# Kernel optimization log

Measured on AMD Instinct MI355X. Metric: run time of the kernel, lower is better.

The kernel has to match this reference:

```python
import jax, jax.numpy as jnp
import numpy as np

CHNN = 1024
K = 2048


def _conv1x1(W, b, x):
    # x: (B, C_in, L), W: (C_out, C_in), b: (C_out,)
    return jnp.einsum('oc,bcl->bol', W, x) + b[None, :, None]


def setup_inputs() -> dict:
    key = jax.random.key(0)
    ks = jax.random.split(key, 10)
    s = 0.02
    return {
        'vc': jax.random.normal(ks[0], (1, CHNN, K), dtype=jnp.float32),
        'vm': jax.random.normal(ks[1], (1, CHNN, K), dtype=jnp.float32),
        'W_ak': jax.random.normal(ks[2], (K, CHNN), dtype=jnp.float32) * s,
        'b_ak': jax.random.normal(ks[3], (K,), dtype=jnp.float32) * s,
        'W_c': jax.random.normal(ks[4], (CHNN, CHNN), dtype=jnp.float32) * s,
        'b_c': jax.random.normal(ks[5], (CHNN,), dtype=jnp.float32) * s,
        'W_mad': jax.random.normal(ks[6], (CHNN, CHNN), dtype=jnp.float32) * s,
        'b_mad': jax.random.normal(ks[7], (CHNN,), dtype=jnp.float32) * s,
        'W_gcn': jax.random.normal(ks[8], (CHNN, CHNN), dtype=jnp.float32) * s,
        'b_gcn': jax.random.normal(ks[9], (CHNN,), dtype=jnp.float32) * s,
    }


def reference(vc, vm, W_ak, b_ak, W_c, b_c, W_mad, b_mad, W_gcn, b_gcn):
    # vcw: (1, K, L) assignment logits; softmax over the K (channel) dim
    vcw = _conv1x1(W_ak, b_ak, vc)
    vcw = jax.nn.softmax(vcw, axis=1)
    w = vcw[0].T                      # (L, K)  (batch forced to 1 by squeeze(0))
    # vm features: (1, CHNN, K)
    vmr = jax.nn.relu(_conv1x1(W_c, b_c, vm))
    # F.linear(vm, w): contract last dim (K) with w's second dim -> (1, CHNN, L)
    vma = jnp.einsum('bck,lk->bcl', vmr, w)
    vma = _conv1x1(W_mad, b_mad, vma)  # (1, CHNN, L)
    # dense adjacency over positions: (1, L, L)
    A = jnp.einsum('bck,bcl->bkl', vma, vma)
    # GCN: x (1, K, CHNN) @ W + b, then softmax(A) @ x  (requires L == K)
    x = jnp.swapaxes(vmr, 1, 2) @ W_gcn + b_gcn
    A = jax.nn.softmax(A, axis=-1)
    out = A @ x                        # (1, L, CHNN)
    return jnp.swapaxes(out, 1, 2)     # (1, CHNN, L)
```

## Files before the change

### kernel.cpp

```cpp
#include <hip/hip_runtime.h>
#include <hip/hip_bf16.h>


typedef __bf16 bf16x4 __attribute__((ext_vector_type(4)));
typedef __bf16 bf16x8 __attribute__((ext_vector_type(8)));
typedef float  f32x4  __attribute__((ext_vector_type(4)));

typedef const void __attribute__((address_space(1)))* gptr_t;
typedef void       __attribute__((address_space(3)))* lptr_t;

__device__ __forceinline__ void load16_lds(const __bf16* g, __bf16* l)
{
    __builtin_amdgcn_global_load_lds((gptr_t)g, (lptr_t)l, 16, 0, 0);
}

#define WAITCNT_VM16 0x4F70
#define WAITCNT_VM8  0x0F78
#define WAITCNT_VM0  0x0F70

template<typename OT, int BIAS_, bool RELU_, int STORE_>
struct GC {
    using OUT_T = OT;
    static constexpr int BIAS = BIAS_, STORE = STORE_;
    static constexpr bool RELU = RELU_;
};

template<class CF>
__device__ __forceinline__ void gemm_body(
    int bid, __bf16* sA, __bf16* sB,
    const __bf16* __restrict__ A, const __bf16* __restrict__ B,
    const float* __restrict__ bias,
    typename CF::OUT_T* __restrict__ C, typename CF::OUT_T* __restrict__ CT,
    int M, int N, int K, int ntx)
{
    const int lane = threadIdx.x & 63;
    const int m0 = (bid / ntx) * 64, n0 = (bid % ntx) * 64;
    const __bf16* gA = A + (size_t)m0 * K;
    const __bf16* gB = B + (size_t)n0 * K;

    f32x4 acc[4][4];
    #pragma unroll
    for (int i = 0; i < 4; ++i)
        #pragma unroll
        for (int j = 0; j < 4; ++j)
            acc[i][j] = (f32x4){0.f, 0.f, 0.f, 0.f};

    auto stage = [&](int k0, int buf) {
        #pragma unroll
        for (int i = 0; i < 4; ++i) {
            const int c = i * 64 + lane;
            const int s = (c ^ (c >> 2) ^ (c >> 4)) & 3;
            load16_lds(gA + (size_t)(c >> 2) * K + k0 + s * 8,
                       &sA[buf * 2048 + i * 512]);
        }
        #pragma unroll
        for (int i = 0; i < 4; ++i) {
            const int c = i * 64 + lane;
            const int s = (c ^ (c >> 2) ^ (c >> 4)) & 3;
            load16_lds(gB + (size_t)(c >> 2) * K + k0 + s * 8,
                       &sB[buf * 2048 + i * 512]);
        }
    };

    const int fsw = ((lane >> 4) ^ lane ^ (lane >> 2)) & 3;

    auto compute = [&](int buf) {
        bf16x8 af[4], bfr[4];
        #pragma unroll
        for (int i = 0; i < 4; ++i) {
            const int off = buf * 2048 + (i * 16 + (lane & 15)) * 32 + fsw * 8;
            af[i]  = *(const bf16x8*)&sA[off];
            bfr[i] = *(const bf16x8*)&sB[off];
        }
        #pragma unroll
        for (int i = 0; i < 4; ++i)
            #pragma unroll
            for (int j = 0; j < 4; ++j)
                acc[i][j] = __builtin_amdgcn_mfma_f32_16x16x32_bf16(af[i], bfr[j], acc[i][j], 0, 0, 0);
    };

    stage(0, 0);
    stage(32, 1);
    stage(64, 2);
    int cur = 0;
    for (int k0 = 0; k0 < K - 96; k0 += 32) {
        __builtin_amdgcn_s_waitcnt(WAITCNT_VM16);
        compute(cur);
        stage(k0 + 96, cur);
        cur = (cur == 2) ? 0 : cur + 1;
    }
    __builtin_amdgcn_s_waitcnt(WAITCNT_VM16);
    compute(cur); cur = (cur == 2) ? 0 : cur + 1;
    __builtin_amdgcn_s_waitcnt(WAITCNT_VM8);
    compute(cur); cur = (cur == 2) ? 0 : cur + 1;
    __builtin_amdgcn_s_waitcnt(WAITCNT_VM0);
    compute(cur);

    #pragma unroll
    for (int i = 0; i < 4; ++i) {
        const int rowb = m0 + i * 16 + (lane >> 4) * 4;
        #pragma unroll
        for (int j = 0; j < 4; ++j) {
            const int col = n0 + j * 16 + (lane & 15);
            f32x4 v = acc[i][j];
            #pragma unroll
            for (int r = 0; r < 4; ++r) {
                float f = v[r];
                if (CF::BIAS == 1) f += bias[rowb + r];
                if (CF::BIAS == 2) f += bias[col];
                if (CF::RELU) f = fmaxf(f, 0.f);
                v[r] = f;
            }
            if (CF::STORE == 0) {
                #pragma unroll
                for (int r = 0; r < 4; ++r)
                    C[(size_t)(rowb + r) * N + col] = (typename CF::OUT_T)v[r];
            } else {
                if constexpr (sizeof(typename CF::OUT_T) == 4) {
                    *(f32x4*)&CT[(size_t)col * M + rowb] = v;
                } else {
                    bf16x4 w = { (__bf16)v[0], (__bf16)v[1], (__bf16)v[2], (__bf16)v[3] };
                    *(bf16x4*)&CT[(size_t)col * M + rowb] = w;
                }
            }
        }
    }
}

__device__ __forceinline__ void softmax_row_w(__bf16* __restrict__ p)
{
    const int lane = threadIdx.x & 63;
    bf16x8 v[4];
    float f[32];
    #pragma unroll
    for (int r = 0; r < 4; ++r)
        v[r] = *(const bf16x8*)&p[(r * 64 + lane) * 8];
    float m = -1e30f;
    #pragma unroll
    for (int r = 0; r < 4; ++r)
        #pragma unroll
        for (int j = 0; j < 8; ++j) {
            f[r * 8 + j] = (float)v[r][j];
            m = fmaxf(m, f[r * 8 + j]);
        }
    #pragma unroll
    for (int s = 1; s < 64; s <<= 1) m = fmaxf(m, __shfl_xor(m, s, 64));
    float sum = 0.f;
    #pragma unroll
    for (int i = 0; i < 32; ++i) { f[i] = expf(f[i] - m); sum += f[i]; }
    #pragma unroll
    for (int s = 1; s < 64; s <<= 1) sum += __shfl_xor(sum, s, 64);
    const float inv = 1.f / sum;
    #pragma unroll
    for (int r = 0; r < 4; ++r) {
        bf16x8 w;
        #pragma unroll
        for (int j = 0; j < 8; ++j) w[j] = (__bf16)(f[r * 8 + j] * inv);
        *(bf16x8*)&p[(r * 64 + lane) * 8] = w;
    }
}

template<class CF>
__global__ __launch_bounds__(64, 2)
void gemm1w(const __bf16* __restrict__ A, const __bf16* __restrict__ B,
            const float* __restrict__ bias,
            typename CF::OUT_T* __restrict__ C, typename CF::OUT_T* __restrict__ CT,
            int M, int N, int K, int ntx)
{
    __shared__ __bf16 sAB[12288];
    gemm_body<CF>(blockIdx.x, sAB, sAB + 6144, A, B, bias, C, CT, M, N, K, ntx);
}

template<class C1, class C2>
__global__ __launch_bounds__(64, 2)
void gemm2w(int nblk1,
            const __bf16* __restrict__ A1, const __bf16* __restrict__ B1,
            const float* __restrict__ b1,
            typename C1::OUT_T* __restrict__ C1p, typename C1::OUT_T* __restrict__ CT1,
            int M1, int N1, int K1, int ntx1,
            const __bf16* __restrict__ A2, const __bf16* __restrict__ B2,
            const float* __restrict__ b2,
            typename C2::OUT_T* __restrict__ C2p, typename C2::OUT_T* __restrict__ CT2,
            int M2, int N2, int K2, int ntx2)
{
    __shared__ __bf16 sAB[12288];
    const int b = blockIdx.x;
    if (b < nblk1)
        gemm_body<C1>(b, sAB, sAB + 6144, A1, B1, b1, C1p, CT1, M1, N1, K1, ntx1);
    else
        gemm_body<C2>(b - nblk1, sAB, sAB + 6144, A2, B2, b2, C2p, CT2, M2, N2, K2, ntx2);
}

template<class C1, class C2>
__global__ __launch_bounds__(64, 2)
void gemm2smw(int nblk1, int nblk2,
              const __bf16* __restrict__ A1, const __bf16* __restrict__ B1,
              const float* __restrict__ b1, typename C1::OUT_T* __restrict__ C1p,
              int M1, int N1, int K1, int ntx1,
              const __bf16* __restrict__ A2, const __bf16* __restrict__ B2,
              const float* __restrict__ b2, typename C2::OUT_T* __restrict__ C2p,
              int M2, int N2, int K2, int ntx2,
              __bf16* __restrict__ SM)
{
    __shared__ __bf16 sAB[12288];
    const int b = blockIdx.x;
    if (b < nblk1)
        gemm_body<C1>(b, sAB, sAB + 6144, A1, B1, b1, C1p,
                      (typename C1::OUT_T*)nullptr, M1, N1, K1, ntx1);
    else if (b < nblk1 + nblk2)
        gemm_body<C2>(b - nblk1, sAB, sAB + 6144, A2, B2, b2, C2p,
                      (typename C2::OUT_T*)nullptr, M2, N2, K2, ntx2);
    else
        softmax_row_w(SM + (size_t)(b - nblk1 - nblk2) * 2048);
}

__global__ __launch_bounds__(64)
void row_softmax_w(__bf16* __restrict__ A)
{
    softmax_row_w(A + (size_t)blockIdx.x * 2048);
}

__device__ __forceinline__ void tp_tile(const float* __restrict__ in,
                                        __bf16* __restrict__ outp,
                                        int R, int C, int bx, int by)
{
    __shared__ float t[32][33];
    const int tx = threadIdx.x & 31, ty = threadIdx.x >> 5;
    #pragma unroll
    for (int i = ty; i < 32; i += 8)
        t[i][tx] = in[(size_t)(by + i) * C + (bx + tx)];
    __syncthreads();
    #pragma unroll
    for (int i = ty; i < 32; i += 8)
        outp[(size_t)(bx + i) * R + (by + tx)] = (__bf16)t[tx][i];
}

__device__ __forceinline__ void cast_blk(const float* __restrict__ s,
                                         __bf16* __restrict__ d, int blk)
{
    const int i = blk * 1024 + threadIdx.x * 4;
    float4 v = *(const float4*)&s[i];
    bf16x4 w = { (__bf16)v.x, (__bf16)v.y, (__bf16)v.z, (__bf16)v.w };
    *(bf16x4*)&d[i] = w;
}

__global__ __launch_bounds__(256)
void prep(const float* __restrict__ vc, __bf16* __restrict__ vcT,
          const float* __restrict__ vm, __bf16* __restrict__ vmT,
          const float* __restrict__ W_ak, __bf16* __restrict__ W_akb,
          const float* __restrict__ W_c, __bf16* __restrict__ W_cb,
          const float* __restrict__ W_mad, __bf16* __restrict__ W_madb,
          const float* __restrict__ W_gcn, __bf16* __restrict__ W_gcnT)
{
    const int x = blockIdx.x;
    if (blockIdx.z == 0) {
        const float* in = (x < 2048) ? vc : vm;
        __bf16* o       = (x < 2048) ? vcT : vmT;
        const int e = x & 2047;
        tp_tile(in, o, 1024, 2048, (e & 63) * 32, (e >> 6) * 32);
    } else if (blockIdx.z == 1) {
        if (x < 2048)      cast_blk(W_ak, W_akb, x);
        else if (x < 3072) cast_blk(W_c, W_cb, x - 2048);
        else               cast_blk(W_mad, W_madb, x - 3072);
    } else {
        if (x >= 1024) return;
        tp_tile(W_gcn, W_gcnT, 1024, 1024, (x & 31) * 32, (x >> 5) * 32);
    }
}

extern "C" void kernel_launch(void* const* d_in, const int* in_sizes, int n_in,
                              void* d_out, int out_size, void* d_ws, size_t ws_size,
                              hipStream_t stream)
{
    const float* vc    = (const float*)d_in[0];
    const float* vm    = (const float*)d_in[1];
    const float* W_ak  = (const float*)d_in[2];
    const float* b_ak  = (const float*)d_in[3];
    const float* W_c   = (const float*)d_in[4];
    const float* b_c   = (const float*)d_in[5];
    const float* W_mad = (const float*)d_in[6];
    const float* b_mad = (const float*)d_in[7];
    const float* W_gcn = (const float*)d_in[8];
    const float* b_gcn = (const float*)d_in[9];
    float* out = (float*)d_out;

    char* ws = (char*)d_ws;
    const size_t MB = 1u << 20;
    __bf16* ST     = (__bf16*)(ws);
    __bf16* P      = (__bf16*)(ws);
    __bf16* vcT    = (__bf16*)(ws + 8 * MB);
    __bf16* vmaT   = (__bf16*)(ws + 8 * MB);
    __bf16* W_akb  = (__bf16*)(ws + 12 * MB);
    __bf16* vmm    = (__bf16*)(ws + 12 * MB);
    __bf16* vmT    = (__bf16*)(ws + 16 * MB);
    __bf16* xT     = (__bf16*)(ws + 16 * MB);
    __bf16* W_cb   = (__bf16*)(ws + 20 * MB);
    __bf16* W_madb = (__bf16*)(ws + 22 * MB);
    __bf16* vmrT   = (__bf16*)(ws + 24 * MB);
    __bf16* W_gcnT = (__bf16*)(ws + 28 * MB);

    using G3  = GC<__bf16, 2, false, 0>;
    using G5  = GC<__bf16, 1, true,  1>;
    using G6  = GC<__bf16, 0, false, 0>;
    using G11 = GC<__bf16, 1, false, 0>;
    using G7  = GC<__bf16, 2, false, 0>;
    using G9  = GC<__bf16, 0, false, 0>;
    using G12 = GC<float,  0, false, 1>;

    prep<<<dim3(4096, 1, 3), 256, 0, stream>>>(vc, vcT, vm, vmT, W_ak, W_akb,
                                               W_c, W_cb, W_mad, W_madb,
                                               W_gcn, W_gcnT);
    gemm2w<G3, G5><<<1536, 64, 0, stream>>>(1024,
        vcT, W_akb, b_ak, ST, (__bf16*)nullptr, 2048, 2048, 1024, 32,
        W_cb, vmT, b_c, (__bf16*)nullptr, vmrT, 1024, 2048, 1024, 32);
    gemm2smw<G6, G11><<<3072, 64, 0, stream>>>(512, 512,
        W_madb, vmrT, nullptr, vmm, 1024, 2048, 1024, 32,
        W_gcnT, vmrT, b_gcn, xT, 1024, 2048, 1024, 32,
        ST);
    gemm1w<G7><<<512, 64, 0, stream>>>(ST, vmm, b_mad, vmaT, (__bf16*)nullptr,
                                       2048, 1024, 2048, 16);
    gemm1w<G9><<<1024, 64, 0, stream>>>(vmaT, vmaT, nullptr, P, (__bf16*)nullptr,
                                        2048, 2048, 1024, 32);
    row_softmax_w<<<2048, 64, 0, stream>>>(P);
    gemm1w<G12><<<512, 64, 0, stream>>>(P, xT, nullptr, (float*)nullptr, out,
                                        2048, 1024, 2048, 16);
}
```

Before: 198.5 us.

## Split-K the two K=2048 GEMMs with fp32 atomic accumulation

The two GEMMs with a 2048-long reduction and only 512 output tiles (the vma projection and the final softmax(A)@x) are split into two K-halves, giving 1024 blocks that accumulate into fp32 buffers with atomic adds. The accumulation buffers are zeroed by extra blocks folded into existing softmax kernels, and a new cast kernel adds the bias and converts the vma partials to bf16. The goal is better occupancy of the device on these GEMMs. The cost is extra fp32 traffic, atomics, one more launch, and a workspace layout where several buffers alias each other.

Measured after the change: 269.1 us. +35.6%, slower.

```diff
diff --git a/kernel.cpp b/kernel.cpp
--- a/kernel.cpp
+++ b/kernel.cpp
@@ -31,12 +31,12 @@
     const __bf16* __restrict__ A, const __bf16* __restrict__ B,
     const float* __restrict__ bias,
     typename CF::OUT_T* __restrict__ C, typename CF::OUT_T* __restrict__ CT,
-    int M, int N, int K, int ntx)
+    int M, int N, int klen, int kstride, int ntx)
 {
     const int lane = threadIdx.x & 63;
     const int m0 = (bid / ntx) * 64, n0 = (bid % ntx) * 64;
-    const __bf16* gA = A + (size_t)m0 * K;
-    const __bf16* gB = B + (size_t)n0 * K;
+    const __bf16* gA = A + (size_t)m0 * kstride;
+    const __bf16* gB = B + (size_t)n0 * kstride;
 
     f32x4 acc[4][4];
     #pragma unroll
@@ -50,14 +50,14 @@
         for (int i = 0; i < 4; ++i) {
             const int c = i * 64 + lane;
             const int s = (c ^ (c >> 2) ^ (c >> 4)) & 3;
-            load16_lds(gA + (size_t)(c >> 2) * K + k0 + s * 8,
+            load16_lds(gA + (size_t)(c >> 2) * kstride + k0 + s * 8,
                        &sA[buf * 2048 + i * 512]);
         }
         #pragma unroll
         for (int i = 0; i < 4; ++i) {
             const int c = i * 64 + lane;
             const int s = (c ^ (c >> 2) ^ (c >> 4)) & 3;
-            load16_lds(gB + (size_t)(c >> 2) * K + k0 + s * 8,
+            load16_lds(gB + (size_t)(c >> 2) * kstride + k0 + s * 8,
                        &sB[buf * 2048 + i * 512]);
         }
     };
@@ -83,7 +83,7 @@
     stage(32, 1);
     stage(64, 2);
     int cur = 0;
-    for (int k0 = 0; k0 < K - 96; k0 += 32) {
+    for (int k0 = 0; k0 < klen - 96; k0 += 32) {
         __builtin_amdgcn_s_waitcnt(WAITCNT_VM16);
         compute(cur);
         stage(k0 + 96, cur);
@@ -106,22 +106,30 @@
             #pragma unroll
             for (int r = 0; r < 4; ++r) {
                 float f = v[r];
-                if (CF::BIAS == 1) f += bias[rowb + r];
-                if (CF::BIAS == 2) f += bias[col];
-                if (CF::RELU) f = fmaxf(f, 0.f);
+                if constexpr (CF::BIAS == 1) f += bias[rowb + r];
+                if constexpr (CF::BIAS == 2) f += bias[col];
+                if constexpr (CF::RELU) f = fmaxf(f, 0.f);
                 v[r] = f;
             }
-            if (CF::STORE == 0) {
+            if constexpr (CF::STORE == 0) {
                 #pragma unroll
                 for (int r = 0; r < 4; ++r)
                     C[(size_t)(rowb + r) * N + col] = (typename CF::OUT_T)v[r];
-            } else {
+            } else if constexpr (CF::STORE == 1) {
                 if constexpr (sizeof(typename CF::OUT_T) == 4) {
                     *(f32x4*)&CT[(size_t)col * M + rowb] = v;
                 } else {
                     bf16x4 w = { (__bf16)v[0], (__bf16)v[1], (__bf16)v[2], (__bf16)v[3] };
                     *(bf16x4*)&CT[(size_t)col * M + rowb] = w;
                 }
+            } else if constexpr (CF::STORE == 2) {
+                #pragma unroll
+                for (int r = 0; r < 4; ++r)
+                    unsafeAtomicAdd((float*)&C[(size_t)(rowb + r) * N + col], v[r]);
+            } else {
+                #pragma unroll
+                for (int r = 0; r < 4; ++r)
+                    unsafeAtomicAdd((float*)&CT[(size_t)col * M + rowb + r], v[r]);
             }
         }
     }
@@ -168,7 +176,28 @@
             int M, int N, int K, int ntx)
 {
     __shared__ __bf16 sAB[12288];
-    gemm_body<CF>(blockIdx.x, sAB, sAB + 6144, A, B, bias, C, CT, M, N, K, ntx);
+    gemm_body<CF>(blockIdx.x, sAB, sAB + 6144, A, B, bias, C, CT, M, N, K, K, ntx);
+}
+
+template<class CF>
+__global__ __launch_bounds__(64, 2)
+void gemm1wks(const __bf16* __restrict__ A, const __bf16* __restrict__ B,
+              float* C0, float* C1, float* C2, float* CT,
+              int M, int N, int K, int ntx, int ntiles)
+{
+    __shared__ __bf16 sAB[12288];
+    const int t = blockIdx.x % ntiles;
+    const int h = blockIdx.x / ntiles;
+    const int kh = K / 2;
+    const int m0 = (t / ntx) * 64;
+    float* C = C0;
+    if (C1) {
+        if (m0 >= 1536)      C = C2 - (size_t)1536 * N;
+        else if (m0 >= 1024) C = C1 - (size_t)1024 * N;
+    }
+    gemm_body<CF>(t, sAB, sAB + 6144, A + h * kh, B + h * kh, nullptr,
+                  (typename CF::OUT_T*)C, (typename CF::OUT_T*)CT,
+                  M, N, kh, K, ntx);
 }
 
 template<class C1, class C2>
@@ -186,9 +215,9 @@
     __shared__ __bf16 sAB[12288];
     const int b = blockIdx.x;
     if (b < nblk1)
-        gemm_body<C1>(b, sAB, sAB + 6144, A1, B1, b1, C1p, CT1, M1, N1, K1, ntx1);
+        gemm_body<C1>(b, sAB, sAB + 6144, A1, B1, b1, C1p, CT1, M1, N1, K1, K1, ntx1);
     else
-        gemm_body<C2>(b - nblk1, sAB, sAB + 6144, A2, B2, b2, C2p, CT2, M2, N2, K2, ntx2);
+        gemm_body<C2>(b - nblk1, sAB, sAB + 6144, A2, B2, b2, C2p, CT2, M2, N2, K2, K2, ntx2);
 }
 
 template<class C1, class C2>
@@ -200,24 +229,67 @@
               const __bf16* __restrict__ A2, const __bf16* __restrict__ B2,
               const float* __restrict__ b2, typename C2::OUT_T* __restrict__ C2p,
               int M2, int N2, int K2, int ntx2,
-              __bf16* __restrict__ SM)
+              __bf16* __restrict__ SM,
+              float* __restrict__ PZ0, float* __restrict__ PZ1,
+              float* __restrict__ PZ2)
 {
     __shared__ __bf16 sAB[12288];
     const int b = blockIdx.x;
     if (b < nblk1)
         gemm_body<C1>(b, sAB, sAB + 6144, A1, B1, b1, C1p,
-                      (typename C1::OUT_T*)nullptr, M1, N1, K1, ntx1);
+                      (typename C1::OUT_T*)nullptr, M1, N1, K1, K1, ntx1);
     else if (b < nblk1 + nblk2)
         gemm_body<C2>(b - nblk1, sAB, sAB + 6144, A2, B2, b2, C2p,
-                      (typename C2::OUT_T*)nullptr, M2, N2, K2, ntx2);
-    else
+                      (typename C2::OUT_T*)nullptr, M2, N2, K2, K2, ntx2);
+    else if (b < nblk1 + nblk2 + 2048)
         softmax_row_w(SM + (size_t)(b - nblk1 - nblk2) * 2048);
+    else {
+        const int r = b - nblk1 - nblk2 - 2048;
+        float* dst = (r < 1024) ? PZ0 + (size_t)r * 1024
+                   : (r < 1536) ? PZ1 + (size_t)(r - 1024) * 1024
+                                : PZ2 + (size_t)(r - 1536) * 1024;
+        const int lane = threadIdx.x & 63;
+        const f32x4 z = {0.f, 0.f, 0.f, 0.f};
+        #pragma unroll
+        for (int j = 0; j < 4; ++j)
+            *(f32x4*)&dst[lane * 16 + j * 4] = z;
+    }
 }
 
 __global__ __launch_bounds__(64)
-void row_softmax_w(__bf16* __restrict__ A)
-{
-    softmax_row_w(A + (size_t)blockIdx.x * 2048);
+void row_softmax_zero(__bf16* __restrict__ A, float* __restrict__ outz)
+{
+    const int b = blockIdx.x;
+    if (b < 2048) {
+        softmax_row_w(A + (size_t)b * 2048);
+    } else {
+        float* dst = outz + (size_t)(b - 2048) * 1024;
+        const int lane = threadIdx.x & 63;
+        const f32x4 z = {0.f, 0.f, 0.f, 0.f};
+        #pragma unroll
+        for (int j = 0; j < 4; ++j)
+            *(f32x4*)&dst[lane * 16 + j * 4] = z;
+    }
+}
+
+__global__ __launch_bounds__(256)
+void part_cast(const float* __restrict__ p0, const float* __restrict__ p1,
+               const float* __restrict__ p2, const float* __restrict__ bias,
+               __bf16* __restrict__ dst)
+{
+    const int r  = blockIdx.x * 4 + (threadIdx.x >> 6);
+    const int c0 = (threadIdx.x & 63) * 16;
+    const float* src = (r < 1024) ? p0 + (size_t)r * 1024
+                     : (r < 1536) ? p1 + (size_t)(r - 1024) * 1024
+                                  : p2 + (size_t)(r - 1536) * 1024;
+    #pragma unroll
+    for (int j = 0; j < 4; ++j) {
+        float4 v  = *(const float4*)&src[c0 + j * 4];
+        float4 bv = *(const float4*)&bias[c0 + j * 4];
+        bf16x4 w = { (__bf16)(v.x + bv.x), (__bf16)(v.y + bv.y),
+                     (__bf16)(v.z + bv.z), (__bf16)(v.w + bv.w) };
+        *(bf16x4*)&dst[(size_t)r * 1024 + c0 + j * 4] = w;
+    }
 }
 
 __device__ __forceinline__ void tp_tile(const float* __restrict__ in,
@@ -289,23 +361,26 @@
     __bf16* ST     = (__bf16*)(ws);
     __bf16* P      = (__bf16*)(ws);
     __bf16* vcT    = (__bf16*)(ws + 8 * MB);
-    __bf16* vmaT   = (__bf16*)(ws + 8 * MB);
+    float*  PZ0    = (float*)(ws + 8 * MB);
     __bf16* W_akb  = (__bf16*)(ws + 12 * MB);
     __bf16* vmm    = (__bf16*)(ws + 12 * MB);
     __bf16* vmT    = (__bf16*)(ws + 16 * MB);
     __bf16* xT     = (__bf16*)(ws + 16 * MB);
     __bf16* W_cb   = (__bf16*)(ws + 20 * MB);
+    float*  PZ1    = (float*)(ws + 20 * MB);
     __bf16* W_madb = (__bf16*)(ws + 22 * MB);
     __bf16* vmrT   = (__bf16*)(ws + 24 * MB);
+    __bf16* vmaT   = (__bf16*)(ws + 24 * MB);
     __bf16* W_gcnT = (__bf16*)(ws + 28 * MB);
-
-    using G3  = GC<__bf16, 2, false, 0>;
-    using G5  = GC<__bf16, 1, true,  1>;
-    using G6  = GC<__bf16, 0, false, 0>;
-    using G11 = GC<__bf16, 1, false, 0>;
-    using G7  = GC<__bf16, 2, false, 0>;
-    using G9  = GC<__bf16, 0, false, 0>;
-    using G12 = GC<float,  0, false, 1>;
+    float*  PZ2    = (float*)(ws + 30 * MB);
+
+    using G3   = GC<__bf16, 2, false, 0>;
+    using G5   = GC<__bf16, 1, true,  1>;
+    using G6   = GC<__bf16, 0, false, 0>;
+    using G11  = GC<__bf16, 1, false, 0>;
+    using G7a  = GC<float,  0, false, 2>;
+    using G9   = GC<__bf16, 0, false, 0>;
+    using G12a = GC<float,  0, false, 3>;
 
     prep<<<dim3(4096, 1, 3), 256, 0, stream>>>(vc, vcT, vm, vmT, W_ak, W_akb,
                                                W_c, W_cb, W_mad, W_madb,
@@ -313,15 +388,18 @@
     gemm2w<G3, G5><<<1536, 64, 0, stream>>>(1024,
         vcT, W_akb, b_ak, ST, (__bf16*)nullptr, 2048, 2048, 1024, 32,
         W_cb, vmT, b_c, (__bf16*)nullptr, vmrT, 1024, 2048, 1024, 32);
-    gemm2smw<G6, G11><<<3072, 64, 0, stream>>>(512, 512,
+    gemm2smw<G6, G11><<<5120, 64, 0, stream>>>(512, 512,
         W_madb, vmrT, nullptr, vmm, 1024, 2048, 1024, 32,
         W_gcnT, vmrT, b_gcn, xT, 1024, 2048, 1024, 32,
-        ST);
-    gemm1w<G7><<<512, 64, 0, stream>>>(ST, vmm, b_mad, vmaT, (__bf16*)nullptr,
-                                       2048, 1024, 2048, 16);
+        ST, PZ0, PZ1, PZ2);
+    gemm1wks<G7a><<<1024, 64, 0, stream>>>(ST, vmm, PZ0, PZ1, PZ2,
+                                           (float*)nullptr,
+                                           2048, 1024, 2048, 16, 512);
+    part_cast<<<512, 256, 0, stream>>>(PZ0, PZ1, PZ2, b_mad, vmaT);
     gemm1w<G9><<<1024, 64, 0, stream>>>(vmaT, vmaT, nullptr, P, (__bf16*)nullptr,
                                         2048, 2048, 1024, 32);
-    row_softmax_w<<<2048, 64, 0, stream>>>(P);
-    gemm1w<G12><<<512, 64, 0, stream>>>(P, xT, nullptr, (float*)nullptr, out,
-                                        2048, 1024, 2048, 16);
-}
+    row_softmax_zero<<<4096, 64, 0, stream>>>(P, out);
+    gemm1wks<G12a><<<1024, 64, 0, stream>>>(P, xT, (float*)nullptr,
+                                            (float*)nullptr, (float*)nullptr,
+                                            out, 2048, 1024, 2048, 16, 512);
+}
```

## Split K in two for the 512-tile GEMMs and reduce partials separately

Applied to the files above, without the earlier changes.

The two GEMMs that launched only 512 single-wave blocks with K=2048 are split along K into two halves, which doubles the block count so more of the device is filled. Each half writes fp32 partials. A new elementwise kernel then sums the partials, adds the bias and casts to bf16 (vma), or adds the second partial into the output. This trades extra fp32 partial traffic and two extra launches for better occupancy.

Result: slower. 220.6 us (+11.1%).

```diff
diff --git a/kernel.cpp b/kernel.cpp
--- a/kernel.cpp
+++ b/kernel.cpp
@@ -31,12 +31,12 @@
     const __bf16* __restrict__ A, const __bf16* __restrict__ B,
     const float* __restrict__ bias,
     typename CF::OUT_T* __restrict__ C, typename CF::OUT_T* __restrict__ CT,
-    int M, int N, int K, int ntx)
+    int M, int N, int klen, int kstride, int ntx)
 {
     const int lane = threadIdx.x & 63;
     const int m0 = (bid / ntx) * 64, n0 = (bid % ntx) * 64;
-    const __bf16* gA = A + (size_t)m0 * K;
-    const __bf16* gB = B + (size_t)n0 * K;
+    const __bf16* gA = A + (size_t)m0 * kstride;
+    const __bf16* gB = B + (size_t)n0 * kstride;
 
     f32x4 acc[4][4];
     #pragma unroll
@@ -50,14 +50,14 @@
         for (int i = 0; i < 4; ++i) {
             const int c = i * 64 + lane;
             const int s = (c ^ (c >> 2) ^ (c >> 4)) & 3;
-            load16_lds(gA + (size_t)(c >> 2) * K + k0 + s * 8,
+            load16_lds(gA + (size_t)(c >> 2) * kstride + k0 + s * 8,
                        &sA[buf * 2048 + i * 512]);
         }
         #pragma unroll
         for (int i = 0; i < 4; ++i) {
             const int c = i * 64 + lane;
             const int s = (c ^ (c >> 2) ^ (c >> 4)) & 3;
-            load16_lds(gB + (size_t)(c >> 2) * K + k0 + s * 8,
+            load16_lds(gB + (size_t)(c >> 2) * kstride + k0 + s * 8,
                        &sB[buf * 2048 + i * 512]);
         }
     };
@@ -83,7 +83,7 @@
     stage(32, 1);
     stage(64, 2);
     int cur = 0;
-    for (int k0 = 0; k0 < K - 96; k0 += 32) {
+    for (int k0 = 0; k0 < klen - 96; k0 += 32) {
         __builtin_amdgcn_s_waitcnt(WAITCNT_VM16);
         compute(cur);
         stage(k0 + 96, cur);
@@ -106,12 +106,12 @@
             #pragma unroll
             for (int r = 0; r < 4; ++r) {
                 float f = v[r];
-                if (CF::BIAS == 1) f += bias[rowb + r];
-                if (CF::BIAS == 2) f += bias[col];
-                if (CF::RELU) f = fmaxf(f, 0.f);
+                if constexpr (CF::BIAS == 1) f += bias[rowb + r];
+                if constexpr (CF::BIAS == 2) f += bias[col];
+                if constexpr (CF::RELU) f = fmaxf(f, 0.f);
                 v[r] = f;
             }
-            if (CF::STORE == 0) {
+            if constexpr (CF::STORE == 0) {
                 #pragma unroll
                 for (int r = 0; r < 4; ++r)
                     C[(size_t)(rowb + r) * N + col] = (typename CF::OUT_T)v[r];
@@ -168,7 +168,22 @@
             int M, int N, int K, int ntx)
 {
     __shared__ __bf16 sAB[12288];
-    gemm_body<CF>(blockIdx.x, sAB, sAB + 6144, A, B, bias, C, CT, M, N, K, ntx);
+    gemm_body<CF>(blockIdx.x, sAB, sAB + 6144, A, B, bias, C, CT, M, N, K, K, ntx);
+}
+
+template<class CF>
+__global__ __launch_bounds__(64, 2)
+void gemm1wks(const __bf16* __restrict__ A, const __bf16* __restrict__ B,
+              typename CF::OUT_T* C0, typename CF::OUT_T* C1,
+              typename CF::OUT_T* CT0, typename CF::OUT_T* CT1,
+              int M, int N, int K, int ntx, int ntiles)
+{
+    __shared__ __bf16 sAB[12288];
+    const int t = blockIdx.x % ntiles;
+    const int h = blockIdx.x / ntiles;
+    const int kh = K / 2;
+    gemm_body<CF>(t, sAB, sAB + 6144, A + (size_t)h * kh, B + (size_t)h * kh,
+                  nullptr, h ? C1 : C0, h ? CT1 : CT0, M, N, kh, K, ntx);
 }
 
 template<class C1, class C2>
@@ -186,9 +201,9 @@
     __shared__ __bf16 sAB[12288];
     const int b = blockIdx.x;
     if (b < nblk1)
-        gemm_body<C1>(b, sAB, sAB + 6144, A1, B1, b1, C1p, CT1, M1, N1, K1, ntx1);
+        gemm_body<C1>(b, sAB, sAB + 6144, A1, B1, b1, C1p, CT1, M1, N1, K1, K1, ntx1);
     else
-        gemm_body<C2>(b - nblk1, sAB, sAB + 6144, A2, B2, b2, C2p, CT2, M2, N2, K2, ntx2);
+        gemm_body<C2>(b - nblk1, sAB, sAB + 6144, A2, B2, b2, C2p, CT2, M2, N2, K2, K2, ntx2);
 }
 
 template<class C1, class C2>
@@ -206,10 +221,10 @@
     const int b = blockIdx.x;
     if (b < nblk1)
         gemm_body<C1>(b, sAB, sAB + 6144, A1, B1, b1, C1p,
-                      (typename C1::OUT_T*)nullptr, M1, N1, K1, ntx1);
+                      (typename C1::OUT_T*)nullptr, M1, N1, K1, K1, ntx1);
     else if (b < nblk1 + nblk2)
         gemm_body<C2>(b - nblk1, sAB, sAB + 6144, A2, B2, b2, C2p,
-                      (typename C2::OUT_T*)nullptr, M2, N2, K2, ntx2);
+                      (typename C2::OUT_T*)nullptr, M2, N2, K2, K2, ntx2);
     else
         softmax_row_w(SM + (size_t)(b - nblk1 - nblk2) * 2048);
 }
@@ -218,6 +233,37 @@
 void row_softmax_w(__bf16* __restrict__ A)
 {
     softmax_row_w(A + (size_t)blockIdx.x * 2048);
+}
+
+__global__ __launch_bounds__(256)
+void part_cast2(const float* __restrict__ pa, const float* __restrict__ pb,
+                const float* __restrict__ bias, __bf16* __restrict__ dst)
+{
+    const int r  = blockIdx.x * 4 + (threadIdx.x >> 6);
+    const int c0 = (threadIdx.x & 63) * 16;
+    const size_t base = (size_t)r * 1024 + c0;
+    #pragma unroll
+    for (int j = 0; j < 4; ++j) {
+        float4 va = *(const float4*)&pa[base + j * 4];
+        float4 vb = *(const float4*)&pb[base + j * 4];
+        float4 bv = *(const float4*)&bias[c0 + j * 4];
+        bf16x4 w = { (__bf16)(va.x + vb.x + bv.x), (__bf16)(va.y + vb.y + bv.y),
+                     (__bf16)(va.z + vb.z + bv.z), (__bf16)(va.w + vb.w + bv.w) };
+        *(bf16x4*)&dst[base + j * 4] = w;
+    }
+}
+
+__global__ __launch_bounds__(256)
+void out_add(float* __restrict__ o, const float* __restrict__ b)
+{
+    const size_t i = ((size_t)blockIdx.x * 256 + threadIdx.x) * 16;
+    #pragma unroll
+    for (int j = 0; j < 4; ++j) {
+        f32x4 va = *(const f32x4*)&o[i + j * 4];
+        f32x4 vb = *(const f32x4*)&b[i + j * 4];
+        va += vb;
+        *(f32x4*)&o[i + j * 4] = va;
+    }
 }
 
 __device__ __forceinline__ void tp_tile(const float* __restrict__ in,
@@ -289,23 +335,26 @@
     __bf16* ST     = (__bf16*)(ws);
     __bf16* P      = (__bf16*)(ws);
     __bf16* vcT    = (__bf16*)(ws + 8 * MB);
-    __bf16* vmaT   = (__bf16*)(ws + 8 * MB);
+    float*  OUTb   = (float*)(ws + 8 * MB);
     __bf16* W_akb  = (__bf16*)(ws + 12 * MB);
     __bf16* vmm    = (__bf16*)(ws + 12 * MB);
     __bf16* vmT    = (__bf16*)(ws + 16 * MB);
     __bf16* xT     = (__bf16*)(ws + 16 * MB);
     __bf16* W_cb   = (__bf16*)(ws + 20 * MB);
+    __bf16* vmaT   = (__bf16*)(ws + 20 * MB);
     __bf16* W_madb = (__bf16*)(ws + 22 * MB);
     __bf16* vmrT   = (__bf16*)(ws + 24 * MB);
+    float*  PA     = (float*)(ws + 24 * MB);
     __bf16* W_gcnT = (__bf16*)(ws + 28 * MB);
-
-    using G3  = GC<__bf16, 2, false, 0>;
-    using G5  = GC<__bf16, 1, true,  1>;
-    using G6  = GC<__bf16, 0, false, 0>;
-    using G11 = GC<__bf16, 1, false, 0>;
-    using G7  = GC<__bf16, 2, false, 0>;
-    using G9  = GC<__bf16, 0, false, 0>;
-    using G12 = GC<float,  0, false, 1>;
+    float*  PB     = (float*)d_out;
+
+    using G3   = GC<__bf16, 2, false, 0>;
+    using G5   = GC<__bf16, 1, true,  1>;
+    using G6   = GC<__bf16, 0, false, 0>;
+    using G11  = GC<__bf16, 1, false, 0>;
+    using G7a  = GC<float,  0, false, 0>;
+    using G9   = GC<__bf16, 0, false, 0>;
+    using G12a = GC<float,  0, false, 1>;
 
     prep<<<dim3(4096, 1, 3), 256, 0, stream>>>(vc, vcT, vm, vmT, W_ak, W_akb,
                                                W_c, W_cb, W_mad, W_madb,
@@ -317,11 +366,15 @@
         W_madb, vmrT, nullptr, vmm, 1024, 2048, 1024, 32,
         W_gcnT, vmrT, b_gcn, xT, 1024, 2048, 1024, 32,
         ST);
-    gemm1w<G7><<<512, 64, 0, stream>>>(ST, vmm, b_mad, vmaT, (__bf16*)nullptr,
-                                       2048, 1024, 2048, 16);
+    gemm1wks<G7a><<<1024, 64, 0, stream>>>(ST, vmm, PA, PB,
+                                           (float*)nullptr, (float*)nullptr,
+                                           2048, 1024, 2048, 16, 512);
+    part_cast2<<<512, 256, 0, stream>>>(PA, PB, b_mad, vmaT);
     gemm1w<G9><<<1024, 64, 0, stream>>>(vmaT, vmaT, nullptr, P, (__bf16*)nullptr,
                                         2048, 2048, 1024, 32);
     row_softmax_w<<<2048, 64, 0, stream>>>(P);
-    gemm1w<G12><<<512, 64, 0, stream>>>(P, xT, nullptr, (float*)nullptr, out,
-                                        2048, 1024, 2048, 16);
-}
+    gemm1wks<G12a><<<1024, 64, 0, stream>>>(P, xT,
+                                            (float*)nullptr, (float*)nullptr,
+                                            out, OUTb, 2048, 1024, 2048, 16, 512);
+    out_add<<<512, 256, 0, stream>>>(out, OUTb);
+}
```

## Use 4-wave 128x128 GEMM tiles with shared LDS staging and barriers

Applied to the files above, without the earlier changes.

The GEMM body changes from one 64x64 tile per single-wave block to a 128x128 tile per 256-thread block. Each wave computes one 64x64 quadrant and loads a quarter of the shared A/B LDS stages. This doubles reuse of each staged operand and halves global traffic per output. The price is a block barrier every k-step, a shallower prefetch (two stages in flight instead of three), and about a quarter as many blocks, which can underfill the CUs on the smaller GEMMs. The fused softmax tail now handles four rows per block, one per wave.

New measurement: 210.8 us. 1.06x slower.

```diff
diff --git a/kernel.cpp b/kernel.cpp
--- a/kernel.cpp
+++ b/kernel.cpp
@@ -14,8 +14,7 @@
     __builtin_amdgcn_global_load_lds((gptr_t)g, (lptr_t)l, 16, 0, 0);
 }
 
-#define WAITCNT_VM16 0x4F70
-#define WAITCNT_VM8  0x0F78
+#define WAITCNT_VM4  0x0F74
 #define WAITCNT_VM0  0x0F70
 
 template<typename OT, int BIAS_, bool RELU_, int STORE_>
@@ -34,9 +33,11 @@
     int M, int N, int K, int ntx)
 {
     const int lane = threadIdx.x & 63;
-    const int m0 = (bid / ntx) * 64, n0 = (bid % ntx) * 64;
-    const __bf16* gA = A + (size_t)m0 * K;
-    const __bf16* gB = B + (size_t)n0 * K;
+    const int w    = threadIdx.x >> 6;
+    const int wr   = w >> 1, wc = w & 1;
+    const int tm0 = (bid / ntx) * 128, tn0 = (bid % ntx) * 128;
+    const __bf16* gA = A + (size_t)tm0 * K;
+    const __bf16* gB = B + (size_t)tn0 * K;
 
     f32x4 acc[4][4];
     #pragma unroll
@@ -47,30 +48,31 @@
 
     auto stage = [&](int k0, int buf) {
         #pragma unroll
-        for (int i = 0; i < 4; ++i) {
-            const int c = i * 64 + lane;
+        for (int ii = 0; ii < 2; ++ii) {
+            const int c = (w * 2 + ii) * 64 + lane;
             const int s = (c ^ (c >> 2) ^ (c >> 4)) & 3;
             load16_lds(gA + (size_t)(c >> 2) * K + k0 + s * 8,
-                       &sA[buf * 2048 + i * 512]);
-        }
-        #pragma unroll
-        for (int i = 0; i < 4; ++i) {
-            const int c = i * 64 + lane;
+                       &sA[buf * 4096 + (w * 2 + ii) * 512]);
+        }
+        #pragma unroll
+        for (int ii = 0; ii < 2; ++ii) {
+            const int c = (w * 2 + ii) * 64 + lane;
             const int s = (c ^ (c >> 2) ^ (c >> 4)) & 3;
             load16_lds(gB + (size_t)(c >> 2) * K + k0 + s * 8,
-                       &sB[buf * 2048 + i * 512]);
+                       &sB[buf * 4096 + (w * 2 + ii) * 512]);
         }
     };
-
-    const int fsw = ((lane >> 4) ^ lane ^ (lane >> 2)) & 3;
 
     auto compute = [&](int buf) {
         bf16x8 af[4], bfr[4];
         #pragma unroll
         for (int i = 0; i < 4; ++i) {
-            const int off = buf * 2048 + (i * 16 + (lane & 15)) * 32 + fsw * 8;
-            af[i]  = *(const bf16x8*)&sA[off];
-            bfr[i] = *(const bf16x8*)&sB[off];
+            const int ra = wr * 64 + i * 16 + (lane & 15);
+            const int sa = ((lane >> 4) ^ ra ^ (ra >> 2)) & 3;
+            af[i] = *(const bf16x8*)&sA[buf * 4096 + ra * 32 + sa * 8];
+            const int rb = wc * 64 + i * 16 + (lane & 15);
+            const int sb = ((lane >> 4) ^ rb ^ (rb >> 2)) & 3;
+            bfr[i] = *(const bf16x8*)&sB[buf * 4096 + rb * 32 + sb * 8];
         }
         #pragma unroll
         for (int i = 0; i < 4; ++i)
@@ -79,23 +81,25 @@
                 acc[i][j] = __builtin_amdgcn_mfma_f32_16x16x32_bf16(af[i], bfr[j], acc[i][j], 0, 0, 0);
     };
 
+    const int ns = K >> 5;
     stage(0, 0);
     stage(32, 1);
-    stage(64, 2);
-    int cur = 0;
-    for (int k0 = 0; k0 < K - 96; k0 += 32) {
-        __builtin_amdgcn_s_waitcnt(WAITCNT_VM16);
+    int cur = 0, st = 2;
+    for (int t = 0; t < ns - 1; ++t) {
+        __builtin_amdgcn_s_waitcnt(WAITCNT_VM4);
+        __builtin_amdgcn_s_barrier();
         compute(cur);
-        stage(k0 + 96, cur);
+        if (t + 2 < ns) {
+            stage((t + 2) * 32, st);
+            st = (st == 2) ? 0 : st + 1;
+        }
         cur = (cur == 2) ? 0 : cur + 1;
     }
-    __builtin_amdgcn_s_waitcnt(WAITCNT_VM16);
-    compute(cur); cur = (cur == 2) ? 0 : cur + 1;
-    __builtin_amdgcn_s_waitcnt(WAITCNT_VM8);
-    compute(cur); cur = (cur == 2) ? 0 : cur + 1;
     __builtin_amdgcn_s_waitcnt(WAITCNT_VM0);
+    __builtin_amdgcn_s_barrier();
     compute(cur);
 
+    const int m0 = tm0 + wr * 64, n0 = tn0 + wc * 64;
     #pragma unroll
     for (int i = 0; i < 4; ++i) {
         const int rowb = m0 + i * 16 + (lane >> 4) * 4;
@@ -106,12 +110,12 @@
             #pragma unroll
             for (int r = 0; r < 4; ++r) {
                 float f = v[r];
-                if (CF::BIAS == 1) f += bias[rowb + r];
-                if (CF::BIAS == 2) f += bias[col];
-                if (CF::RELU) f = fmaxf(f, 0.f);
+                if constexpr (CF::BIAS == 1) f += bias[rowb + r];
+                if constexpr (CF::BIAS == 2) f += bias[col];
+                if constexpr (CF::RELU) f = fmaxf(f, 0.f);
                 v[r] = f;
             }
-            if (CF::STORE == 0) {
+            if constexpr (CF::STORE == 0) {
                 #pragma unroll
                 for (int r = 0; r < 4; ++r)
                     C[(size_t)(rowb + r) * N + col] = (typename CF::OUT_T)v[r];
@@ -119,8 +123,8 @@
                 if constexpr (sizeof(typename CF::OUT_T) == 4) {
                     *(f32x4*)&CT[(size_t)col * M + rowb] = v;
                 } else {
-                    bf16x4 w = { (__bf16)v[0], (__bf16)v[1], (__bf16)v[2], (__bf16)v[3] };
-                    *(bf16x4*)&CT[(size_t)col * M + rowb] = w;
+                    bf16x4 wv = { (__bf16)v[0], (__bf16)v[1], (__bf16)v[2], (__bf16)v[3] };
+                    *(bf16x4*)&CT[(size_t)col * M + rowb] = wv;
                 }
             }
         }
@@ -153,26 +157,26 @@
     const float inv = 1.f / sum;
     #pragma unroll
     for (int r = 0; r < 4; ++r) {
-        bf16x8 w;
-        #pragma unroll
-        for (int j = 0; j < 8; ++j) w[j] = (__bf16)(f[r * 8 + j] * inv);
-        *(bf16x8*)&p[(r * 64 + lane) * 8] = w;
+        bf16x8 wv;
+        #pragma unroll
+        for (int j = 0; j < 8; ++j) wv[j] = (__bf16)(f[r * 8 + j] * inv);
+        *(bf16x8*)&p[(r * 64 + lane) * 8] = wv;
     }
 }
 
 template<class CF>
-__global__ __launch_bounds__(64, 2)
+__global__ __launch_bounds__(256, 2)
 void gemm1w(const __bf16* __restrict__ A, const __bf16* __restrict__ B,
             const float* __restrict__ bias,
             typename CF::OUT_T* __restrict__ C, typename CF::OUT_T* __restrict__ CT,
             int M, int N, int K, int ntx)
 {
-    __shared__ __bf16 sAB[12288];
-    gemm_body<CF>(blockIdx.x, sAB, sAB + 6144, A, B, bias, C, CT, M, N, K, ntx);
+    __shared__ __bf16 sAB[24576];
+    gemm_body<CF>(blockIdx.x, sAB, sAB + 12288, A, B, bias, C, CT, M, N, K, ntx);
 }
 
 template<class C1, class C2>
-__global__ __launch_bounds__(64, 2)
+__global__ __launch_bounds__(256, 2)
 void gemm2w(int nblk1,
             const __bf16* __restrict__ A1, const __bf16* __restrict__ B1,
             const float* __restrict__ b1,
@@ -183,16 +187,16 @@
             typename C2::OUT_T* __restrict__ C2p, typename C2::OUT_T* __restrict__ CT2,
             int M2, int N2, int K2, int ntx2)
 {
-    __shared__ __bf16 sAB[12288];
+    __shared__ __bf16 sAB[24576];
     const int b = blockIdx.x;
     if (b < nblk1)
-        gemm_body<C1>(b, sAB, sAB + 6144, A1, B1, b1, C1p, CT1, M1, N1, K1, ntx1);
+        gemm_body<C1>(b, sAB, sAB + 12288, A1, B1, b1, C1p, CT1, M1, N1, K1, ntx1);
     else
-        gemm_body<C2>(b - nblk1, sAB, sAB + 6144, A2, B2, b2, C2p, CT2, M2, N2, K2, ntx2);
+        gemm_body<C2>(b - nblk1, sAB, sAB + 12288, A2, B2, b2, C2p, CT2, M2, N2, K2, ntx2);
 }
 
 template<class C1, class C2>
-__global__ __launch_bounds__(64, 2)
+__global__ __launch_bounds__(256, 2)
 void gemm2smw(int nblk1, int nblk2,
               const __bf16* __restrict__ A1, const __bf16* __restrict__ B1,
               const float* __restrict__ b1, typename C1::OUT_T* __restrict__ C1p,
@@ -202,16 +206,18 @@
               int M2, int N2, int K2, int ntx2,
               __bf16* __restrict__ SM)
 {
-    __shared__ __bf16 sAB[12288];
+    __shared__ __bf16 sAB[24576];
     const int b = blockIdx.x;
     if (b < nblk1)
-        gemm_body<C1>(b, sAB, sAB + 6144, A1, B1, b1, C1p,
+        gemm_body<C1>(b, sAB, sAB + 12288, A1, B1, b1, C1p,
                       (typename C1::OUT_T*)nullptr, M1, N1, K1, ntx1);
     else if (b < nblk1 + nblk2)
-        gemm_body<C2>(b - nblk1, sAB, sAB + 6144, A2, B2, b2, C2p,
+        gemm_body<C2>(b - nblk1, sAB, sAB + 12288, A2, B2, b2, C2p,
                       (typename C2::OUT_T*)nullptr, M2, N2, K2, ntx2);
-    else
-        softmax_row_w(SM + (size_t)(b - nblk1 - nblk2) * 2048);
+    else {
+        const int row = (b - nblk1 - nblk2) * 4 + (threadIdx.x >> 6);
+        softmax_row_w(SM + (size_t)row * 2048);
+    }
 }
 
 __global__ __launch_bounds__(64)
@@ -310,18 +316,18 @@
     prep<<<dim3(4096, 1, 3), 256, 0, stream>>>(vc, vcT, vm, vmT, W_ak, W_akb,
                                                W_c, W_cb, W_mad, W_madb,
                                                W_gcn, W_gcnT);
-    gemm2w<G3, G5><<<1536, 64, 0, stream>>>(1024,
-        vcT, W_akb, b_ak, ST, (__bf16*)nullptr, 2048, 2048, 1024, 32,
-        W_cb, vmT, b_c, (__bf16*)nullptr, vmrT, 1024, 2048, 1024, 32);
-    gemm2smw<G6, G11><<<3072, 64, 0, stream>>>(512, 512,
-        W_madb, vmrT, nullptr, vmm, 1024, 2048, 1024, 32,
-        W_gcnT, vmrT, b_gcn, xT, 1024, 2048, 1024, 32,
+    gemm2w<G3, G5><<<384, 256, 0, stream>>>(256,
+        vcT, W_akb, b_ak, ST, (__bf16*)nullptr, 2048, 2048, 1024, 16,
+        W_cb, vmT, b_c, (__bf16*)nullptr, vmrT, 1024, 2048, 1024, 16);
+    gemm2smw<G6, G11><<<768, 256, 0, stream>>>(128, 128,
+        W_madb, vmrT, nullptr, vmm, 1024, 2048, 1024, 16,
+        W_gcnT, vmrT, b_gcn, xT, 1024, 2048, 1024, 16,
         ST);
-    gemm1w<G7><<<512, 64, 0, stream>>>(ST, vmm, b_mad, vmaT, (__bf16*)nullptr,
-                                       2048, 1024, 2048, 16);
-    gemm1w<G9><<<1024, 64, 0, stream>>>(vmaT, vmaT, nullptr, P, (__bf16*)nullptr,
-                                        2048, 2048, 1024, 32);
+    gemm1w<G7><<<128, 256, 0, stream>>>(ST, vmm, b_mad, vmaT, (__bf16*)nullptr,
+                                        2048, 1024, 2048, 8);
+    gemm1w<G9><<<256, 256, 0, stream>>>(vmaT, vmaT, nullptr, P, (__bf16*)nullptr,
+                                        2048, 2048, 1024, 16);
     row_softmax_w<<<2048, 64, 0, stream>>>(P);
-    gemm1w<G12><<<512, 64, 0, stream>>>(P, xT, nullptr, (float*)nullptr, out,
-                                        2048, 1024, 2048, 16);
-}
+    gemm1w<G12><<<128, 256, 0, stream>>>(P, xT, nullptr, (float*)nullptr, out,
+                                         2048, 1024, 2048, 8);
+}
```
